# Kernel optimization log

Measured on AMD Instinct MI355X. Metric: run time of the kernel, lower is better.

The kernel has to match this reference:

```python
import jax, jax.numpy as jnp
import numpy as np

N_NODES = 100000
N_EDGES = 1600000
IN_CH, HID_CH, OUT_CH, NCLASS = 128, 256, 256, 40


def gcn_conv(x, edge_index, edge_weight, W, b):
    """PyG GCNConv: h = D^{-1/2} (A + I) D^{-1/2} (x @ W) + b, weighted edges."""
    n = x.shape[0]
    row, col = edge_index[0], edge_index[1]
    loop = jnp.arange(n)
    row = jnp.concatenate([row, loop])
    col = jnp.concatenate([col, loop])
    ew = jnp.concatenate([edge_weight, jnp.ones((n,), x.dtype)])  # self-loop weight 1
    deg = jax.ops.segment_sum(ew, col, num_segments=n)
    dinv = jnp.where(deg > 0, jax.lax.rsqrt(deg), 0.0)
    norm = dinv[row] * ew * dinv[col]            # [E+N]
    h = x @ W                                    # transform before propagate (as PyG)
    msg = h[row] * norm[:, None]                 # gather + scale, [E+N, F]
    out = jax.ops.segment_sum(msg, col, num_segments=n)  # scatter-add
    return out + b


def setup_inputs() -> dict:
    key = jax.random.key(0)
    ks = jax.random.split(key, 9)
    x = jax.random.normal(ks[0], (N_NODES, IN_CH), dtype=jnp.float32)
    edge_index = jax.random.randint(ks[1], (2, N_EDGES), 0, N_NODES, dtype=jnp.int64)
    edge_attr = jax.random.uniform(ks[2], (N_EDGES,), dtype=jnp.float32)
    s1 = 1.0 / np.sqrt(IN_CH)
    s2 = 1.0 / np.sqrt(HID_CH)
    s3 = 1.0 / np.sqrt(OUT_CH)
    W1 = jax.random.uniform(ks[3], (IN_CH, HID_CH), jnp.float32, -s1, s1)
    b1 = jnp.zeros((HID_CH,), jnp.float32)
    W2 = jax.random.uniform(ks[4], (HID_CH, OUT_CH), jnp.float32, -s2, s2)
    b2 = jnp.zeros((OUT_CH,), jnp.float32)
    fcW = jax.random.uniform(ks[5], (OUT_CH, NCLASS), jnp.float32, -s3, s3)
    fcb = jax.random.uniform(ks[6], (NCLASS,), jnp.float32, -s3, s3)
    return {"x": x, "edge_index": edge_index, "edge_attr": edge_attr,
            "W1": W1, "b1": b1, "W2": W2, "b2": b2, "fcW": fcW, "fcb": fcb}


def reference(x, edge_index, edge_attr, W1, b1, W2, b2, fcW, fcb):
    # eval mode: dropout is identity
    h = jax.nn.relu(gcn_conv(x, edge_index, edge_attr, W1, b1))
    h = jax.nn.relu(gcn_conv(h, edge_index, edge_attr, W2, b2))
    return h @ fcW + fcb
```

## Files before the change

kernel.cpp:

```cpp
#include <hip/hip_runtime.h>

#define NODES 100000
#define EDGES 1600000

typedef __attribute__((ext_vector_type(4))) float floatx4;
typedef _Float16 h16;
typedef __attribute__((ext_vector_type(2))) _Float16 h16x2;
typedef __attribute__((ext_vector_type(4))) _Float16 h16x4;
typedef __attribute__((ext_vector_type(8))) _Float16 h16x8;
typedef __attribute__((ext_vector_type(8))) _Float16 half8;

#define WSCALE 64.0f
#define WINV   (1.0f / 64.0f)

__device__ inline void load_lds16(void* lds, const void* g) {
    __builtin_amdgcn_global_load_lds((const __attribute__((address_space(1))) void*)g,
                                     (__attribute__((address_space(3))) void*)lds, 16, 0, 0);
}

__global__ __launch_bounds__(256) void k_init(unsigned long long* __restrict__ packed, int n) {
    int i = blockIdx.x * 256 + threadIdx.x;
    if (i < n) packed[i] = 0ull;
}

__device__ inline void w_split(const float* W, h16* Wh, h16* Wl, int idx, int K) {
    int k = idx >> 8, nn = idx & 255;
    float v = W[idx] * WSCALE;
    h16 h = (h16)v;
    h16 l = (h16)(v - (float)h);
    Wh[nn * K + k] = h;
    Wl[nn * K + k] = l;
}

__global__ __launch_bounds__(256) void k_hist(unsigned long long* __restrict__ packed,
                                              unsigned short* __restrict__ rank,
                                              const int* __restrict__ col,
                                              const float* __restrict__ ew, int e,
                                              const float* __restrict__ W1, h16* __restrict__ W1h, h16* __restrict__ W1l,
                                              const float* __restrict__ W2, h16* __restrict__ W2h, h16* __restrict__ W2l,
                                              const float* __restrict__ x, h16* __restrict__ x16, int n) {
    int b = blockIdx.x;
    if (b < 6250) {
        int i = b * 256 + threadIdx.x;
        if (i < e) {
            int c = col[i];
            unsigned long long v = (1ull << 40) |
                (unsigned long long)__float2uint_rn(ew[i] * 1048576.0f);
            unsigned long long old = atomicAdd(&packed[c], v);
            rank[i] = (unsigned short)(old >> 40);
        }
    } else if (b < 6378) {
        w_split(W1, W1h, W1l, (b - 6250) * 256 + threadIdx.x, 128);
    } else if (b < 6634) {
        w_split(W2, W2h, W2l, (b - 6378) * 256 + threadIdx.x, 256);
    } else {
        int i = (b - 6634) * 256 + threadIdx.x;
        if (i < n * 32) {
            float4 v = reinterpret_cast<const float4*>(x)[i];
            h16x4 h;
            h.x = (h16)v.x; h.y = (h16)v.y; h.z = (h16)v.z; h.w = (h16)v.w;
            reinterpret_cast<h16x4*>(x16)[i] = h;
        }
    }
}

__global__ __launch_bounds__(256) void k_scan1(const unsigned long long* __restrict__ packed,
                                               int* __restrict__ rowptr,
                                               int* __restrict__ partials,
                                               float* __restrict__ dinv, int n) {
    __shared__ int wtot[4];
    const int tid = threadIdx.x, lane = tid & 63, wid = tid >> 6;
    int i = blockIdx.x * 256 + tid;
    int v = 0;
    if (i < n) {
        unsigned long long p = packed[i];
        v = (int)(p >> 40);
        float deg = 1.0f + (float)(p & 0xFFFFFFFFFFull) * (1.0f / 1048576.0f);
        dinv[i] = rsqrtf(deg);
    }
    int incl = v;
#pragma unroll
    for (int off = 1; off < 64; off <<= 1) {
        int t = __shfl_up(incl, off, 64);
        if (lane >= off) incl += t;
    }
    if (lane == 63) wtot[wid] = incl;
    __syncthreads();
    int woff = 0;
    for (int k = 0; k < wid; ++k) woff += wtot[k];
    if (i < n) rowptr[i] = woff + incl - v;
    if (tid == 255) partials[blockIdx.x] = woff + incl;
}

__global__ __launch_bounds__(512) void k_scan2(int* __restrict__ partials, int nb) {
    __shared__ int wtot[8];
    const int tid = threadIdx.x, lane = tid & 63, wid = tid >> 6;
    int v = (tid < nb) ? partials[tid] : 0;
    int incl = v;
#pragma unroll
    for (int off = 1; off < 64; off <<= 1) {
        int t = __shfl_up(incl, off, 64);
        if (lane >= off) incl += t;
    }
    if (lane == 63) wtot[wid] = incl;
    __syncthreads();
    int woff = 0;
    for (int k = 0; k < wid; ++k) woff += wtot[k];
    if (tid < nb) partials[tid] = woff + incl - v;
}

__global__ __launch_bounds__(256) void k_scan3(int* __restrict__ rowptr,
                                               const int* __restrict__ partials, int n) {
    int i = blockIdx.x * 256 + threadIdx.x;
    if (i < n) rowptr[i] += partials[blockIdx.x];
    if (blockIdx.x == 0 && threadIdx.x == 0) rowptr[n] = EDGES;
}

__global__ __launch_bounds__(256) void k_build(const int* __restrict__ rowptr,
                                               const unsigned short* __restrict__ rank,
                                               int2* __restrict__ meta,
                                               const int* __restrict__ row, const int* __restrict__ col,
                                               const float* __restrict__ ew,
                                               const float* __restrict__ dinv, int e) {
    int i = blockIdx.x * 256 + threadIdx.x;
    if (i >= e) return;
    int r = row[i], c = col[i];
    float w = dinv[r] * ew[i] * dinv[c];
    int pos = rowptr[c] + rank[i];
    meta[pos] = make_int2(r, __float_as_int(w));
}

__global__ __launch_bounds__(256) void k_gather_x(h16* __restrict__ Xa,
                                                  const h16* __restrict__ x16,
                                                  const float* __restrict__ dinv,
                                                  const int* __restrict__ rowptr,
                                                  const int2* __restrict__ meta, int n) {
    int node = (blockIdx.x << 2) + (threadIdx.x >> 6);
    if (node >= n) return;
    const int lane = threadIdx.x & 63;
    const int j = lane << 1;
    float di = dinv[node];
    float s = di * di;
    h16x2 xs = *reinterpret_cast<const h16x2*>(x16 + (size_t)node * 128 + j);
    float2 a0 = make_float2((float)xs.x * s, (float)xs.y * s);
    float2 a1 = make_float2(0.f, 0.f);

    int p = rowptr[node];
    const int end = rowptr[node + 1];
    for (; p + 3 < end; p += 4) {
        int2 m0 = meta[p],     m1 = meta[p + 1];
        int2 m2 = meta[p + 2], m3 = meta[p + 3];
        h16x2 h0 = *reinterpret_cast<const h16x2*>(x16 + (size_t)m0.x * 128 + j);
        h16x2 h1 = *reinterpret_cast<const h16x2*>(x16 + (size_t)m1.x * 128 + j);
        h16x2 h2 = *reinterpret_cast<const h16x2*>(x16 + (size_t)m2.x * 128 + j);
        h16x2 h3 = *reinterpret_cast<const h16x2*>(x16 + (size_t)m3.x * 128 + j);
        float w0 = __int_as_float(m0.y), w1 = __int_as_float(m1.y);
        float w2 = __int_as_float(m2.y), w3 = __int_as_float(m3.y);
        a0.x = fmaf((float)h0.x, w0, a0.x); a0.y = fmaf((float)h0.y, w0, a0.y);
        a1.x = fmaf((float)h1.x, w1, a1.x); a1.y = fmaf((float)h1.y, w1, a1.y);
        a0.x = fmaf((float)h2.x, w2, a0.x); a0.y = fmaf((float)h2.y, w2, a0.y);
        a1.x = fmaf((float)h3.x, w3, a1.x); a1.y = fmaf((float)h3.y, w3, a1.y);
    }
    for (; p < end; ++p) {
        int2 m0 = meta[p];
        h16x2 h0 = *reinterpret_cast<const h16x2*>(x16 + (size_t)m0.x * 128 + j);
        float w0 = __int_as_float(m0.y);
        a0.x = fmaf((float)h0.x, w0, a0.x); a0.y = fmaf((float)h0.y, w0, a0.y);
    }
    a0.x += a1.x; a0.y += a1.y;

    h16x2 o;
    o.x = (h16)a0.x; o.y = (h16)a0.y;
    *reinterpret_cast<h16x2*>(Xa + (size_t)node * 128 + j) = o;
}

__global__ __launch_bounds__(256) void k_gather(h16* __restrict__ P,
                                                const h16* __restrict__ H,
                                                const float* __restrict__ dinv,
                                                const int* __restrict__ rowptr,
                                                const int2* __restrict__ meta,
                                                const float* __restrict__ bias, int n) {
    int node = (blockIdx.x << 2) + (threadIdx.x >> 6);
    if (node >= n) return;
    const int lane = threadIdx.x & 63;
    const int j = lane << 2;
    float di = dinv[node];
    float s = di * di;
    float4 b = *reinterpret_cast<const float4*>(bias + j);
    h16x4 hv = *reinterpret_cast<const h16x4*>(H + (size_t)node * 256 + j);
    float4 acc;
    acc.x = fmaf((float)hv.x, s, b.x); acc.y = fmaf((float)hv.y, s, b.y);
    acc.z = fmaf((float)hv.z, s, b.z); acc.w = fmaf((float)hv.w, s, b.w);
    float4 acc2 = make_float4(0.f, 0.f, 0.f, 0.f);

    int p = rowptr[node];
    const int end = rowptr[node + 1];
    for (; p + 3 < end; p += 4) {
        int2 m0 = meta[p],     m1 = meta[p + 1];
        int2 m2 = meta[p + 2], m3 = meta[p + 3];
        h16x4 h0 = *reinterpret_cast<const h16x4*>(H + (size_t)m0.x * 256 + j);
        h16x4 h1 = *reinterpret_cast<const h16x4*>(H + (size_t)m1.x * 256 + j);
        h16x4 h2 = *reinterpret_cast<const h16x4*>(H + (size_t)m2.x * 256 + j);
        h16x4 h3 = *reinterpret_cast<const h16x4*>(H + (size_t)m3.x * 256 + j);
        float w0 = __int_as_float(m0.y), w1 = __int_as_float(m1.y);
        float w2 = __int_as_float(m2.y), w3 = __int_as_float(m3.y);
        acc.x  = fmaf((float)h0.x, w0, acc.x);  acc.y  = fmaf((float)h0.y, w0, acc.y);
        acc.z  = fmaf((float)h0.z, w0, acc.z);  acc.w  = fmaf((float)h0.w, w0, acc.w);
        acc2.x = fmaf((float)h1.x, w1, acc2.x); acc2.y = fmaf((float)h1.y, w1, acc2.y);
        acc2.z = fmaf((float)h1.z, w1, acc2.z); acc2.w = fmaf((float)h1.w, w1, acc2.w);
        acc.x  = fmaf((float)h2.x, w2, acc.x);  acc.y  = fmaf((float)h2.y, w2, acc.y);
        acc.z  = fmaf((float)h2.z, w2, acc.z);  acc.w  = fmaf((float)h2.w, w2, acc.w);
        acc2.x = fmaf((float)h3.x, w3, acc2.x); acc2.y = fmaf((float)h3.y, w3, acc2.y);
        acc2.z = fmaf((float)h3.z, w3, acc2.z); acc2.w = fmaf((float)h3.w, w3, acc2.w);
    }
    for (; p < end; ++p) {
        int2 m0 = meta[p];
        h16x4 h0 = *reinterpret_cast<const h16x4*>(H + (size_t)m0.x * 256 + j);
        float w0 = __int_as_float(m0.y);
        acc.x = fmaf((float)h0.x, w0, acc.x); acc.y = fmaf((float)h0.y, w0, acc.y);
        acc.z = fmaf((float)h0.z, w0, acc.z); acc.w = fmaf((float)h0.w, w0, acc.w);
    }
    acc.x += acc2.x; acc.y += acc2.y; acc.z += acc2.z; acc.w += acc2.w;

    h16x4 o;
    o.x = (h16)fmaxf(acc.x, 0.f); o.y = (h16)fmaxf(acc.y, 0.f);
    o.z = (h16)fmaxf(acc.z, 0.f); o.w = (h16)fmaxf(acc.w, 0.f);
    *reinterpret_cast<h16x4*>(P + (size_t)node * 256 + j) = o;
}

template<bool SPLIT>
__global__ __launch_bounds__(256) void k_gemm_f16(const h16* __restrict__ Ag,
                                                  const h16* __restrict__ Bhg,
                                                  const h16* __restrict__ Blg,
                                                  h16* __restrict__ Out,
                                                  const float* __restrict__ bias,
                                                  int M, int K) {
    __shared__ __attribute__((aligned(16))) char ldsA[8192];
    __shared__ __attribute__((aligned(16))) char ldsBh[8192];
    __shared__ __attribute__((aligned(16))) char ldsBl[8192];
    const int tid = threadIdx.x;
    const int lane = tid & 63, wid = tid >> 6;
    const int quad = lane >> 4, l16 = lane & 15;
    const int rowBase = blockIdx.x * 128;
    const int colBase = blockIdx.y * 128;
    const int wm = (wid & 1) * 64, wn = (wid >> 1) * 64;

    floatx4 acc[4][4] = {};

    const int c0 = wid * 64 + lane;
    const int c1 = c0 + 256;
    const int r0 = ((c0 >> 6) << 4) + (c0 & 15), q0 = (c0 >> 4) & 3;
    const int r1 = ((c1 >> 6) << 4) + (c1 & 15), q1 = (c1 >> 4) & 3;
    const size_t aoff0 = (size_t)(rowBase + r0) * K + q0 * 8;
    const size_t aoff1 = (size_t)(rowBase + r1) * K + q1 * 8;
    const size_t boff0 = (size_t)(colBase + r0) * K + q0 * 8;
    const size_t boff1 = (size_t)(colBase + r1) * K + q1 * 8;
    const int lo0 = (wid * 64) * 16;
    const int lo1 = (256 + wid * 64) * 16;

    for (int k0 = 0; k0 < K; k0 += 32) {
        load_lds16(ldsA + lo0, Ag + aoff0 + k0);
        load_lds16(ldsA + lo1, Ag + aoff1 + k0);
        load_lds16(ldsBh + lo0, Bhg + boff0 + k0);
        load_lds16(ldsBh + lo1, Bhg + boff1 + k0);
        load_lds16(ldsBl + lo0, Blg + boff0 + k0);
        load_lds16(ldsBl + lo1, Blg + boff1 + k0);
        __syncthreads();

        const half8* vA  = (const half8*)ldsA;
        const half8* vBh = (const half8*)ldsBh;
        const half8* vBl = (const half8*)ldsBl;
        half8 af[4], bfh[4], bfl[4];
#pragma unroll
        for (int mi = 0; mi < 4; ++mi)
            af[mi] = vA[((wm >> 4) + mi) * 64 + quad * 16 + l16];
#pragma unroll
        for (int ni = 0; ni < 4; ++ni) {
            int idx = ((wn >> 4) + ni) * 64 + quad * 16 + l16;
            bfh[ni] = vBh[idx];
            bfl[ni] = vBl[idx];
        }
#pragma unroll
        for (int mi = 0; mi < 4; ++mi)
#pragma unroll
            for (int ni = 0; ni < 4; ++ni) {
                acc[mi][ni] = __builtin_amdgcn_mfma_f32_16x16x32_f16(af[mi], bfh[ni], acc[mi][ni], 0, 0, 0);
                acc[mi][ni] = __builtin_amdgcn_mfma_f32_16x16x32_f16(af[mi], bfl[ni], acc[mi][ni], 0, 0, 0);
            }
        __syncthreads();
    }

#pragma unroll
    for (int mi = 0; mi < 4; ++mi) {
#pragma unroll
        for (int r = 0; r < 4; ++r) {
            int grow = rowBase + wm + mi * 16 + quad * 4 + r;
            if (grow < M) {
#pragma unroll
                for (int ni = 0; ni < 4; ++ni) {
                    int gcol = colBase + wn + ni * 16 + l16;
                    float v = acc[mi][ni][r] * WINV;
                    if (SPLIT) v = fmaxf(v + bias[gcol], 0.f);
                    Out[(size_t)grow * 256 + gcol] = (h16)v;
                }
            }
        }
    }
}

__global__ __launch_bounds__(256) void k_fc(float* __restrict__ out, const h16* __restrict__ X,
                                            const float* __restrict__ W, const float* __restrict__ bias,
                                            int M) {
    __shared__ float Ws[256 * 40];
    __shared__ float Xs[32][69];
    const int tid = threadIdx.x;
#pragma unroll
    for (int t = 0; t < 10; ++t) {
        int idx = (t * 256 + tid) * 4;
        *reinterpret_cast<float4*>(&Ws[idx]) = *reinterpret_cast<const float4*>(W + idx);
    }
    const int rowBase = blockIdx.x * 64;
    const int r  = tid >> 2;
    const int cg = (tid & 3) * 10;
    const int kq = (tid & 3) << 3;
    float acc[10] = {};

    for (int k0 = 0; k0 < 256; k0 += 32) {
        int rr = rowBase + r;
        h16x8 v = {};
        if (rr < M) v = *reinterpret_cast<const h16x8*>(X + (size_t)rr * 256 + k0 + kq);
#pragma unroll
        for (int j = 0; j < 8; ++j) Xs[kq + j][r] = (float)v[j];
        __syncthreads();
#pragma unroll
        for (int kk = 0; kk < 32; ++kk) {
            float xv = Xs[kk][r];
#pragma unroll
            for (int j = 0; j < 10; ++j)
                acc[j] = fmaf(xv, Ws[(k0 + kk) * 40 + cg + j], acc[j]);
        }
        __syncthreads();
    }

    int orow = rowBase + r;
    if (orow < M) {
#pragma unroll
        for (int j = 0; j < 10; ++j)
            out[(size_t)orow * 40 + cg + j] = acc[j] + bias[cg + j];
    }
}

extern "C" void kernel_launch(void* const* d_in, const int* in_sizes, int n_in,
                              void* d_out, int out_size, void* d_ws, size_t ws_size,
                              hipStream_t stream) {
    const float* x   = (const float*)d_in[0];
    const int*   ei  = (const int*)d_in[1];
    const float* ea  = (const float*)d_in[2];
    const float* W1  = (const float*)d_in[3];
    const float* b1  = (const float*)d_in[4];
    const float* W2  = (const float*)d_in[5];
    const float* b2  = (const float*)d_in[6];
    const float* fcW = (const float*)d_in[7];
    const float* fcb = (const float*)d_in[8];
    float* out = (float*)d_out;

    const int n = NODES, e = EDGES;
    const int* row = ei;
    const int* col = ei + e;

    char* ws = (char*)d_ws;
    char*  Areg   = ws;
    char*  Breg   = ws + 102400000u;
    float* dinv   = (float*)(ws + 204800000u);
    unsigned long long* packed = (unsigned long long*)(ws + 205200000u);
    int*   rowptr = (int*)  (ws + 206000000u);
    int2*  meta   = (int2*) (ws + 206400016u);
    h16*   W1h    = (h16*)  (ws + 219200016u);
    h16*   W1l    = (h16*)  (ws + 219265552u);
    h16*   W2h    = (h16*)  (ws + 219331088u);
    h16*   W2l    = (h16*)  (ws + 219462160u);

    int* partials = (int*)Areg;
    h16* Xa16 = (h16*)Areg;
    h16* x16  = (h16*)(Areg + 25600000u);
    h16* H2h  = (h16*)Areg;
    unsigned short* rank = (unsigned short*)Breg;
    h16* P1   = (h16*)Breg;
    h16* P2h  = (h16*)(Breg + 51200000u);

    const int nb = (n + 255) / 256;
    const int eb = e / 256;

    k_init<<<nb, 256, 0, stream>>>(packed, n);
    k_hist<<<19134, 256, 0, stream>>>(packed, rank, col, ea, e,
                                      W1, W1h, W1l, W2, W2h, W2l, x, x16, n);
    k_scan1<<<nb, 256, 0, stream>>>(packed, rowptr, partials, dinv, n);
    k_scan2<<<1, 512, 0, stream>>>(partials, nb);
    k_scan3<<<nb, 256, 0, stream>>>(rowptr, partials, n);
    k_build<<<eb, 256, 0, stream>>>(rowptr, rank, meta, row, col, ea, dinv, e);

    dim3 gg((n + 127) / 128, 2);

    k_gather_x<<<(n + 3) / 4, 256, 0, stream>>>(Xa16, x16, dinv, rowptr, meta, n);
    k_gemm_f16<true><<<gg, 256, 0, stream>>>(Xa16, W1h, W1l, P1, b1, n, 128);

    k_gemm_f16<false><<<gg, 256, 0, stream>>>(P1, W2h, W2l, H2h, nullptr, n, 256);
    k_gather<<<(n + 3) / 4, 256, 0, stream>>>(P2h, H2h, dinv, rowptr, meta, b2, n);

    k_fc<<<(n + 63) / 64, 256, 0, stream>>>(out, P2h, fcW, fcb, n);
}
```

Before: 614.5 us.

## Aggregate before second GEMM, fuse GEMM2 with FC, pack edge metadata

Layer 2 now aggregates P1 over the graph first and then applies W2, using the associativity A(HW)=(AH)W. This lets the second GEMM be fused with bias, ReLU and the final FC layer in one kernel that stages the tile in LDS, which removes the H2/P2 round trips and the separate k_fc launch. Edge metadata is packed into 32 bits (15-bit fp16 weight plus source index), halving meta traffic. The gather kernels split edges across half-waves and use wider vector loads. Risks: reduced weight precision, 17 bits for the node index, and the large LDS footprint of the fused kernel lowering occupancy.

```diff
diff --git a/kernel.cpp b/kernel.cpp
--- a/kernel.cpp
+++ b/kernel.cpp
@@ -5,7 +5,6 @@
 
 typedef __attribute__((ext_vector_type(4))) float floatx4;
 typedef _Float16 h16;
-typedef __attribute__((ext_vector_type(2))) _Float16 h16x2;
 typedef __attribute__((ext_vector_type(4))) _Float16 h16x4;
 typedef __attribute__((ext_vector_type(8))) _Float16 h16x8;
 typedef __attribute__((ext_vector_type(8))) _Float16 half8;
@@ -16,6 +15,10 @@
 __device__ inline void load_lds16(void* lds, const void* g) {
     __builtin_amdgcn_global_load_lds((const __attribute__((address_space(1))) void*)g,
                                      (__attribute__((address_space(3))) void*)lds, 16, 0, 0);
+}
+
+__device__ inline float meta_w(unsigned m) {
+    return (float)__builtin_bit_cast(h16, (unsigned short)(m & 0x7FFFu));
 }
 
 __global__ __launch_bounds__(256) void k_init(unsigned long long* __restrict__ packed, int n) {
@@ -118,7 +121,7 @@
 
 __global__ __launch_bounds__(256) void k_build(const int* __restrict__ rowptr,
                                                const unsigned short* __restrict__ rank,
-                                               int2* __restrict__ meta,
+                                               unsigned* __restrict__ meta,
                                                const int* __restrict__ row, const int* __restrict__ col,
                                                const float* __restrict__ ew,
                                                const float* __restrict__ dinv, int e) {
@@ -126,115 +129,120 @@
     if (i >= e) return;
     int r = row[i], c = col[i];
     float w = dinv[r] * ew[i] * dinv[c];
-    int pos = rowptr[c] + rank[i];
-    meta[pos] = make_int2(r, __float_as_int(w));
+    unsigned short wb = __builtin_bit_cast(unsigned short, (h16)w);
+    meta[rowptr[c] + rank[i]] = ((unsigned)r << 15) | wb;
 }
 
 __global__ __launch_bounds__(256) void k_gather_x(h16* __restrict__ Xa,
                                                   const h16* __restrict__ x16,
                                                   const float* __restrict__ dinv,
                                                   const int* __restrict__ rowptr,
-                                                  const int2* __restrict__ meta, int n) {
+                                                  const unsigned* __restrict__ meta, int n) {
     int node = (blockIdx.x << 2) + (threadIdx.x >> 6);
     if (node >= n) return;
     const int lane = threadIdx.x & 63;
-    const int j = lane << 1;
-    float di = dinv[node];
-    float s = di * di;
-    h16x2 xs = *reinterpret_cast<const h16x2*>(x16 + (size_t)node * 128 + j);
-    float2 a0 = make_float2((float)xs.x * s, (float)xs.y * s);
-    float2 a1 = make_float2(0.f, 0.f);
-
+    const int half = lane >> 5;
+    const int cb = (lane & 31) << 2;
+    float a0[4] = {}, a1[4] = {};
     int p = rowptr[node];
     const int end = rowptr[node + 1];
     for (; p + 3 < end; p += 4) {
-        int2 m0 = meta[p],     m1 = meta[p + 1];
-        int2 m2 = meta[p + 2], m3 = meta[p + 3];
-        h16x2 h0 = *reinterpret_cast<const h16x2*>(x16 + (size_t)m0.x * 128 + j);
-        h16x2 h1 = *reinterpret_cast<const h16x2*>(x16 + (size_t)m1.x * 128 + j);
-        h16x2 h2 = *reinterpret_cast<const h16x2*>(x16 + (size_t)m2.x * 128 + j);
-        h16x2 h3 = *reinterpret_cast<const h16x2*>(x16 + (size_t)m3.x * 128 + j);
-        float w0 = __int_as_float(m0.y), w1 = __int_as_float(m1.y);
-        float w2 = __int_as_float(m2.y), w3 = __int_as_float(m3.y);
-        a0.x = fmaf((float)h0.x, w0, a0.x); a0.y = fmaf((float)h0.y, w0, a0.y);
-        a1.x = fmaf((float)h1.x, w1, a1.x); a1.y = fmaf((float)h1.y, w1, a1.y);
-        a0.x = fmaf((float)h2.x, w2, a0.x); a0.y = fmaf((float)h2.y, w2, a0.y);
-        a1.x = fmaf((float)h3.x, w3, a1.x); a1.y = fmaf((float)h3.y, w3, a1.y);
-    }
-    for (; p < end; ++p) {
-        int2 m0 = meta[p];
-        h16x2 h0 = *reinterpret_cast<const h16x2*>(x16 + (size_t)m0.x * 128 + j);
-        float w0 = __int_as_float(m0.y);
-        a0.x = fmaf((float)h0.x, w0, a0.x); a0.y = fmaf((float)h0.y, w0, a0.y);
-    }
-    a0.x += a1.x; a0.y += a1.y;
-
-    h16x2 o;
-    o.x = (h16)a0.x; o.y = (h16)a0.y;
-    *reinterpret_cast<h16x2*>(Xa + (size_t)node * 128 + j) = o;
-}
-
-__global__ __launch_bounds__(256) void k_gather(h16* __restrict__ P,
-                                                const h16* __restrict__ H,
-                                                const float* __restrict__ dinv,
-                                                const int* __restrict__ rowptr,
-                                                const int2* __restrict__ meta,
-                                                const float* __restrict__ bias, int n) {
+        unsigned m0 = meta[p + half], m1 = meta[p + half + 2];
+        h16x4 h0 = *(const h16x4*)(x16 + (size_t)(m0 >> 15) * 128 + cb);
+        h16x4 h1 = *(const h16x4*)(x16 + (size_t)(m1 >> 15) * 128 + cb);
+        float w0 = meta_w(m0), w1 = meta_w(m1);
+#pragma unroll
+        for (int j = 0; j < 4; ++j) {
+            a0[j] = fmaf((float)h0[j], w0, a0[j]);
+            a1[j] = fmaf((float)h1[j], w1, a1[j]);
+        }
+    }
+    for (; p + 1 < end; p += 2) {
+        unsigned m0 = meta[p + half];
+        h16x4 h0 = *(const h16x4*)(x16 + (size_t)(m0 >> 15) * 128 + cb);
+        float w0 = meta_w(m0);
+#pragma unroll
+        for (int j = 0; j < 4; ++j) a0[j] = fmaf((float)h0[j], w0, a0[j]);
+    }
+    if (half == 0 && p < end) {
+        unsigned m0 = meta[p];
+        h16x4 h0 = *(const h16x4*)(x16 + (size_t)(m0 >> 15) * 128 + cb);
+        float w0 = meta_w(m0);
+#pragma unroll
+        for (int j = 0; j < 4; ++j) a1[j] = fmaf((float)h0[j], w0, a1[j]);
+    }
+#pragma unroll
+    for (int j = 0; j < 4; ++j) a0[j] += a1[j];
+#pragma unroll
+    for (int j = 0; j < 4; ++j) a0[j] += __shfl(a0[j], lane + 32);
+    if (half == 0) {
+        float s = dinv[node]; s = s * s;
+        h16x4 sv = *(const h16x4*)(x16 + (size_t)node * 128 + cb);
+        h16x4 o;
+#pragma unroll
+        for (int j = 0; j < 4; ++j) o[j] = (h16)fmaf((float)sv[j], s, a0[j]);
+        *(h16x4*)(Xa + (size_t)node * 128 + cb) = o;
+    }
+}
+
+__global__ __launch_bounds__(256) void k_gather_y(h16* __restrict__ Y,
+                                                  const h16* __restrict__ P1,
+                                                  const float* __restrict__ dinv,
+                                                  const int* __restrict__ rowptr,
+                                                  const unsigned* __restrict__ meta, int n) {
     int node = (blockIdx.x << 2) + (threadIdx.x >> 6);
     if (node >= n) return;
     const int lane = threadIdx.x & 63;
-    const int j = lane << 2;
-    float di = dinv[node];
-    float s = di * di;
-    float4 b = *reinterpret_cast<const float4*>(bias + j);
-    h16x4 hv = *reinterpret_cast<const h16x4*>(H + (size_t)node * 256 + j);
-    float4 acc;
-    acc.x = fmaf((float)hv.x, s, b.x); acc.y = fmaf((float)hv.y, s, b.y);
-    acc.z = fmaf((float)hv.z, s, b.z); acc.w = fmaf((float)hv.w, s, b.w);
-    float4 acc2 = make_float4(0.f, 0.f, 0.f, 0.f);
-
+    const int half = lane >> 5;
+    const int cb = (lane & 31) << 3;
+    float a0[8] = {}, a1[8] = {};
     int p = rowptr[node];
     const int end = rowptr[node + 1];
     for (; p + 3 < end; p += 4) {
-        int2 m0 = meta[p],     m1 = meta[p + 1];
-        int2 m2 = meta[p + 2], m3 = meta[p + 3];
-        h16x4 h0 = *reinterpret_cast<const h16x4*>(H + (size_t)m0.x * 256 + j);
-        h16x4 h1 = *reinterpret_cast<const h16x4*>(H + (size_t)m1.x * 256 + j);
-        h16x4 h2 = *reinterpret_cast<const h16x4*>(H + (size_t)m2.x * 256 + j);
-        h16x4 h3 = *reinterpret_cast<const h16x4*>(H + (size_t)m3.x * 256 + j);
-        float w0 = __int_as_float(m0.y), w1 = __int_as_float(m1.y);
-        float w2 = __int_as_float(m2.y), w3 = __int_as_float(m3.y);
-        acc.x  = fmaf((float)h0.x, w0, acc.x);  acc.y  = fmaf((float)h0.y, w0, acc.y);
-        acc.z  = fmaf((float)h0.z, w0, acc.z);  acc.w  = fmaf((float)h0.w, w0, acc.w);
-        acc2.x = fmaf((float)h1.x, w1, acc2.x); acc2.y = fmaf((float)h1.y, w1, acc2.y);
-        acc2.z = fmaf((float)h1.z, w1, acc2.z); acc2.w = fmaf((float)h1.w, w1, acc2.w);
-        acc.x  = fmaf((float)h2.x, w2, acc.x);  acc.y  = fmaf((float)h2.y, w2, acc.y);
-        acc.z  = fmaf((float)h2.z, w2, acc.z);  acc.w  = fmaf((float)h2.w, w2, acc.w);
-        acc2.x = fmaf((float)h3.x, w3, acc2.x); acc2.y = fmaf((float)h3.y, w3, acc2.y);
-        acc2.z = fmaf((float)h3.z, w3, acc2.z); acc2.w = fmaf((float)h3.w, w3, acc2.w);
-    }
-    for (; p < end; ++p) {
-        int2 m0 = meta[p];
-        h16x4 h0 = *reinterpret_cast<const h16x4*>(H + (size_t)m0.x * 256 + j);
-        float w0 = __int_as_float(m0.y);
-        acc.x = fmaf((float)h0.x, w0, acc.x); acc.y = fmaf((float)h0.y, w0, acc.y);
-        acc.z = fmaf((float)h0.z, w0, acc.z); acc.w = fmaf((float)h0.w, w0, acc.w);
-    }
-    acc.x += acc2.x; acc.y += acc2.y; acc.z += acc2.z; acc.w += acc2.w;
-
-    h16x4 o;
-    o.x = (h16)fmaxf(acc.x, 0.f); o.y = (h16)fmaxf(acc.y, 0.f);
-    o.z = (h16)fmaxf(acc.z, 0.f); o.w = (h16)fmaxf(acc.w, 0.f);
-    *reinterpret_cast<h16x4*>(P + (size_t)node * 256 + j) = o;
-}
-
-template<bool SPLIT>
-__global__ __launch_bounds__(256) void k_gemm_f16(const h16* __restrict__ Ag,
-                                                  const h16* __restrict__ Bhg,
-                                                  const h16* __restrict__ Blg,
-                                                  h16* __restrict__ Out,
-                                                  const float* __restrict__ bias,
-                                                  int M, int K) {
+        unsigned m0 = meta[p + half], m1 = meta[p + half + 2];
+        h16x8 h0 = *(const h16x8*)(P1 + (size_t)(m0 >> 15) * 256 + cb);
+        h16x8 h1 = *(const h16x8*)(P1 + (size_t)(m1 >> 15) * 256 + cb);
+        float w0 = meta_w(m0), w1 = meta_w(m1);
+#pragma unroll
+        for (int j = 0; j < 8; ++j) {
+            a0[j] = fmaf((float)h0[j], w0, a0[j]);
+            a1[j] = fmaf((float)h1[j], w1, a1[j]);
+        }
+    }
+    for (; p + 1 < end; p += 2) {
+        unsigned m0 = meta[p + half];
+        h16x8 h0 = *(const h16x8*)(P1 + (size_t)(m0 >> 15) * 256 + cb);
+        float w0 = meta_w(m0);
+#pragma unroll
+        for (int j = 0; j < 8; ++j) a0[j] = fmaf((float)h0[j], w0, a0[j]);
+    }
+    if (half == 0 && p < end) {
+        unsigned m0 = meta[p];
+        h16x8 h0 = *(const h16x8*)(P1 + (size_t)(m0 >> 15) * 256 + cb);
+        float w0 = meta_w(m0);
+#pragma unroll
+        for (int j = 0; j < 8; ++j) a1[j] = fmaf((float)h0[j], w0, a1[j]);
+    }
+#pragma unroll
+    for (int j = 0; j < 8; ++j) a0[j] += a1[j];
+#pragma unroll
+    for (int j = 0; j < 8; ++j) a0[j] += __shfl(a0[j], lane + 32);
+    if (half == 0) {
+        float s = dinv[node]; s = s * s;
+        h16x8 sv = *(const h16x8*)(P1 + (size_t)node * 256 + cb);
+        h16x8 o;
+#pragma unroll
+        for (int j = 0; j < 8; ++j) o[j] = (h16)fmaf((float)sv[j], s, a0[j]);
+        *(h16x8*)(Y + (size_t)node * 256 + cb) = o;
+    }
+}
+
+__global__ __launch_bounds__(256) void k_gemm1(const h16* __restrict__ Ag,
+                                               const h16* __restrict__ Bhg,
+                                               const h16* __restrict__ Blg,
+                                               h16* __restrict__ Out,
+                                               const float* __restrict__ bias,
+                                               int M, int K) {
     __shared__ __attribute__((aligned(16))) char ldsA[8192];
     __shared__ __attribute__((aligned(16))) char ldsBh[8192];
     __shared__ __attribute__((aligned(16))) char ldsBl[8192];
@@ -299,8 +307,7 @@
 #pragma unroll
                 for (int ni = 0; ni < 4; ++ni) {
                     int gcol = colBase + wn + ni * 16 + l16;
-                    float v = acc[mi][ni][r] * WINV;
-                    if (SPLIT) v = fmaxf(v + bias[gcol], 0.f);
+                    float v = fmaxf(acc[mi][ni][r] * WINV + bias[gcol], 0.f);
                     Out[(size_t)grow * 256 + gcol] = (h16)v;
                 }
             }
@@ -308,45 +315,99 @@
     }
 }
 
-__global__ __launch_bounds__(256) void k_fc(float* __restrict__ out, const h16* __restrict__ X,
-                                            const float* __restrict__ W, const float* __restrict__ bias,
-                                            int M) {
-    __shared__ float Ws[256 * 40];
-    __shared__ float Xs[32][69];
+__global__ __launch_bounds__(256, 2) void k_gemm2fc(const h16* __restrict__ Y,
+                                                    const h16* __restrict__ Bhg,
+                                                    const h16* __restrict__ Blg,
+                                                    const float* __restrict__ b2,
+                                                    const float* __restrict__ fcW,
+                                                    const float* __restrict__ fcb,
+                                                    float* __restrict__ out, int M) {
+    __shared__ __attribute__((aligned(16))) char lds[67584];
+    char* ldsA  = lds;
+    char* ldsBh = lds + 8192;
+    char* ldsBl = lds + 24576;
     const int tid = threadIdx.x;
-#pragma unroll
-    for (int t = 0; t < 10; ++t) {
-        int idx = (t * 256 + tid) * 4;
-        *reinterpret_cast<float4*>(&Ws[idx]) = *reinterpret_cast<const float4*>(W + idx);
-    }
-    const int rowBase = blockIdx.x * 64;
-    const int r  = tid >> 2;
-    const int cg = (tid & 3) * 10;
-    const int kq = (tid & 3) << 3;
-    float acc[10] = {};
+    const int lane = tid & 63, wid = tid >> 6;
+    const int quad = lane >> 4, l16 = lane & 15;
+    const int rowBase = blockIdx.x * 128;
+    const int wm = (wid & 1) * 64, wn = (wid >> 1) * 128;
+
+    floatx4 acc[4][8] = {};
 
     for (int k0 = 0; k0 < 256; k0 += 32) {
-        int rr = rowBase + r;
-        h16x8 v = {};
-        if (rr < M) v = *reinterpret_cast<const h16x8*>(X + (size_t)rr * 256 + k0 + kq);
-#pragma unroll
-        for (int j = 0; j < 8; ++j) Xs[kq + j][r] = (float)v[j];
+#pragma unroll
+        for (int i = 0; i < 2; ++i) {
+            int c = tid + i * 256;
+            int r = ((c >> 6) << 4) + (c & 15), q = (c >> 4) & 3;
+            load_lds16(ldsA + c * 16, Y + (size_t)(rowBase + r) * 256 + k0 + q * 8);
+        }
+#pragma unroll
+        for (int i = 0; i < 4; ++i) {
+            int c = tid + i * 256;
+            int r = ((c >> 6) << 4) + (c & 15), q = (c >> 4) & 3;
+            size_t go = (size_t)r * 256 + k0 + q * 8;
+            load_lds16(ldsBh + c * 16, Bhg + go);
+            load_lds16(ldsBl + c * 16, Blg + go);
+        }
         __syncthreads();
-#pragma unroll
-        for (int kk = 0; kk < 32; ++kk) {
-            float xv = Xs[kk][r];
-#pragma unroll
-            for (int j = 0; j < 10; ++j)
-                acc[j] = fmaf(xv, Ws[(k0 + kk) * 40 + cg + j], acc[j]);
+
+        const half8* vA  = (const half8*)ldsA;
+        const half8* vBh = (const half8*)ldsBh;
+        const half8* vBl = (const half8*)ldsBl;
+        half8 af[4];
+#pragma unroll
+        for (int mi = 0; mi < 4; ++mi)
+            af[mi] = vA[((wm >> 4) + mi) * 64 + quad * 16 + l16];
+#pragma unroll
+        for (int ni = 0; ni < 8; ++ni) {
+            int bidx = ((wn >> 4) + ni) * 64 + quad * 16 + l16;
+            half8 bh = vBh[bidx];
+            half8 bl = vBl[bidx];
+#pragma unroll
+            for (int mi = 0; mi < 4; ++mi) {
+                acc[mi][ni] = __builtin_amdgcn_mfma_f32_16x16x32_f16(af[mi], bh, acc[mi][ni], 0, 0, 0);
+                acc[mi][ni] = __builtin_amdgcn_mfma_f32_16x16x32_f16(af[mi], bl, acc[mi][ni], 0, 0, 0);
+            }
         }
         __syncthreads();
     }
 
-    int orow = rowBase + r;
-    if (orow < M) {
-#pragma unroll
-        for (int j = 0; j < 10; ++j)
-            out[(size_t)orow * 40 + cg + j] = acc[j] + bias[cg + j];
+    h16* P2s = (h16*)lds;
+#pragma unroll
+    for (int mi = 0; mi < 4; ++mi)
+#pragma unroll
+        for (int r = 0; r < 4; ++r) {
+            int lrow = wm + mi * 16 + quad * 4 + r;
+#pragma unroll
+            for (int ni = 0; ni < 8; ++ni) {
+                int col = wn + ni * 16 + l16;
+                float v = fmaxf(acc[mi][ni][r] * WINV + b2[col], 0.f);
+                P2s[lrow * 264 + col] = (h16)v;
+            }
+        }
+    __syncthreads();
+
+    const int myrow = (wid & 1) * 64 + lane;
+    const int jb = (wid >> 1) * 20;
+    const int grow = rowBase + myrow;
+    float fa[20] = {};
+    for (int kc = 0; kc < 32; ++kc) {
+        h16x8 xv8 = *(const h16x8*)(P2s + myrow * 264 + kc * 8);
+        float xv[8];
+#pragma unroll
+        for (int j = 0; j < 8; ++j) xv[j] = (float)xv8[j];
+#pragma unroll
+        for (int kk = 0; kk < 8; ++kk) {
+            const float* wrow = fcW + (kc * 8 + kk) * 40 + jb;
+#pragma unroll
+            for (int j = 0; j < 20; ++j)
+                fa[j] = fmaf(xv[kk], wrow[j], fa[j]);
+        }
+    }
+    if (grow < M) {
+#pragma unroll
+        for (int j = 0; j < 20; ++j)
+            out[(size_t)grow * 40 + jb + j] = fa[j] + fcb[jb + j];
     }
 }
 
@@ -374,19 +435,18 @@
     float* dinv   = (float*)(ws + 204800000u);
     unsigned long long* packed = (unsigned long long*)(ws + 205200000u);
     int*   rowptr = (int*)  (ws + 206000000u);
-    int2*  meta   = (int2*) (ws + 206400016u);
-    h16*   W1h    = (h16*)  (ws + 219200016u);
-    h16*   W1l    = (h16*)  (ws + 219265552u);
-    h16*   W2h    = (h16*)  (ws + 219331088u);
-    h16*   W2l    = (h16*)  (ws + 219462160u);
+    unsigned* meta = (unsigned*)(ws + 206400016u);
+    h16*   W1h    = (h16*)  (ws + 212800016u);
+    h16*   W1l    = (h16*)  (ws + 212865552u);
+    h16*   W2h    = (h16*)  (ws + 212931088u);
+    h16*   W2l    = (h16*)  (ws + 213062160u);
 
     int* partials = (int*)Areg;
     h16* Xa16 = (h16*)Areg;
     h16* x16  = (h16*)(Areg + 25600000u);
-    h16* H2h  = (h16*)Areg;
+    h16* Yh   = (h16*)Areg;
     unsigned short* rank = (unsigned short*)Breg;
     h16* P1   = (h16*)Breg;
-    h16* P2h  = (h16*)(Breg + 51200000u);
 
     const int nb = (n + 255) / 256;
     const int eb = e / 256;
@@ -399,13 +459,10 @@
     k_scan3<<<nb, 256, 0, stream>>>(rowptr, partials, n);
     k_build<<<eb, 256, 0, stream>>>(rowptr, rank, meta, row, col, ea, dinv, e);
 
+    k_gather_x<<<(n + 3) / 4, 256, 0, stream>>>(Xa16, x16, dinv, rowptr, meta, n);
     dim3 gg((n + 127) / 128, 2);
-
-    k_gather_x<<<(n + 3) / 4, 256, 0, stream>>>(Xa16, x16, dinv, rowptr, meta, n);
-    k_gemm_f16<true><<<gg, 256, 0, stream>>>(Xa16, W1h, W1l, P1, b1, n, 128);
-
-    k_gemm_f16<false><<<gg, 256, 0, stream>>>(P1, W2h, W2l, H2h, nullptr, n, 256);
-    k_gather<<<(n + 3) / 4, 256, 0, stream>>>(P2h, H2h, dinv, rowptr, meta, b2, n);
-
-    k_fc<<<(n + 63) / 64, 256, 0, stream>>>(out, P2h, fcW, fcb, n);
-}
+    k_gemm1<<<gg, 256, 0, stream>>>(Xa16, W1h, W1l, P1, b1, n, 128);
+
+    k_gather_y<<<(n + 3) / 4, 256, 0, stream>>>(Yh, P1, dinv, rowptr, meta, n);
+    k_gemm2fc<<<(n + 127) / 128, 256, 0, stream>>>(Yh, W2h, W2l, b2, fcW, fcb, out, n);
+}
```

Measured after the change: 664.5 us. +8.1%, slower.
